# Performance work log

Hardware: AMD Instinct MI355X
Metric: run time of the kernel (lower is better)

The kernel has to match this reference:

```python
import jax, jax.numpy as jnp
import numpy as np

N, E, IN, HID, OUT, H = 50000, 400000, 128, 32, 64, 4
HID_DIM = HID * H  # 128


def _param(key, shape, scale=0.05):
    return jax.random.normal(key, shape, dtype=jnp.float32) * scale


def setup_inputs() -> dict:
    key = jax.random.key(0)
    ks = jax.random.split(key, 32)
    inp = {
        "x": jax.random.normal(ks[0], (N, IN), dtype=jnp.float32),
        "edge_index": jax.random.randint(ks[1], (2, E), 0, N, dtype=jnp.int32),
        "edge_weight": jax.random.uniform(ks[2], (E,), dtype=jnp.float32),
        # layer 0: in=128 -> H=4, C=32, concat => 128
        "Wl0": _param(ks[3], (IN, H * HID)), "bl0": jnp.zeros((H * HID,), jnp.float32),
        "Wr0": _param(ks[4], (IN, H * HID)), "br0": jnp.zeros((H * HID,), jnp.float32),
        "We0": _param(ks[5], (1, H * HID)),
        "att0": _param(ks[6], (H, HID)),
        "b0": jnp.zeros((H * HID,), jnp.float32),
        "g0": jnp.ones((H * HID,), jnp.float32), "be0": jnp.zeros((H * HID,), jnp.float32),
        # layer 1: in=128 -> H=4, C=64, concat=False (mean over heads) => 64
        "Wl1": _param(ks[7], (HID_DIM, H * OUT)), "bl1": jnp.zeros((H * OUT,), jnp.float32),
        "Wr1": _param(ks[8], (HID_DIM, H * OUT)), "br1": jnp.zeros((H * OUT,), jnp.float32),
        "We1": _param(ks[9], (1, H * OUT)),
        "att1": _param(ks[10], (H, OUT)),
        "b1": jnp.zeros((OUT,), jnp.float32),
        "g1": jnp.ones((OUT,), jnp.float32), "be1": jnp.zeros((OUT,), jnp.float32),
        # residual projections
        "P0": _param(ks[11], (IN, HID_DIM)), "pb0": jnp.zeros((HID_DIM,), jnp.float32),
        "P1": _param(ks[12], (HID_DIM, OUT)), "pb1": jnp.zeros((OUT,), jnp.float32),
    }
    return inp


def _add_self_loops(src, dst, ew):
    # PyG add_self_loops with fill_value='mean': loop attr = mean of incoming edge attrs per node
    s = jax.ops.segment_sum(ew, dst, num_segments=N)
    cnt = jax.ops.segment_sum(jnp.ones_like(ew), dst, num_segments=N)
    loop_w = s / jnp.maximum(cnt, 1.0)
    idx = jnp.arange(N, dtype=src.dtype)
    return jnp.concatenate([src, idx]), jnp.concatenate([dst, idx]), jnp.concatenate([ew, loop_w])


def _gatv2_layer(x, src, dst, ew, Wl, bl, Wr, br, We, att, b, g, be, C, concat):
    xl = (x @ Wl + bl).reshape(N, H, C)  # source transform (lin_l)
    xr = (x @ Wr + br).reshape(N, H, C)  # target transform (lin_r)
    eattr = (ew[:, None] @ We).reshape(-1, H, C)
    e = jax.nn.leaky_relu(xl[src] + xr[dst] + eattr, 0.2)  # [E', H, C]
    logits = jnp.einsum('ehc,hc->eh', e, att)
    # segment softmax over target nodes
    m = jax.ops.segment_max(logits, dst, num_segments=N)
    p = jnp.exp(logits - m[dst])
    denom = jax.ops.segment_sum(p, dst, num_segments=N)
    alpha = p / denom[dst]
    out = jax.ops.segment_sum(xl[src] * alpha[..., None], dst, num_segments=N)  # [N, H, C]
    if concat:
        out = out.reshape(N, H * C) + b
    else:
        out = out.mean(axis=1) + b
    out = jax.nn.elu(out)
    mu = out.mean(-1, keepdims=True)
    var = out.var(-1, keepdims=True)
    return (out - mu) / jnp.sqrt(var + 1e-5) * g + be


def reference(x, edge_index, edge_weight,
              Wl0, bl0, Wr0, br0, We0, att0, b0, g0, be0,
              Wl1, bl1, Wr1, br1, We1, att1, b1, g1, be1,
              P0, pb0, P1, pb1):
    src, dst, ew = _add_self_loops(edge_index[0], edge_index[1], edge_weight)
    h = x
    h1 = _gatv2_layer(h, src, dst, ew, Wl0, bl0, Wr0, br0, We0, att0, b0, g0, be0, HID, True)
    h = h1 + (h @ P0 + pb0)
    h2 = _gatv2_layer(h, src, dst, ew, Wl1, bl1, Wr1, br1, We1, att1, b1, g1, be1, OUT, False)
    h = h2 + (h @ P1 + pb1)
    return h
```

## Files before the change

### kernel.cpp

```cpp
#include <hip/hip_runtime.h>
#include <math.h>

#define N_NODES 50000
#define N_EDGES 400000
#define NPAD    50176
#define MROWS   50048
#define HC0 128
#define HC1 256

typedef short bf16x8 __attribute__((ext_vector_type(8)));
typedef float f32x4  __attribute__((ext_vector_type(4)));

__device__ inline unsigned short f2bf(float f) {
  union { float f; unsigned u; } v; v.f = f;
  unsigned r = v.u + 0x7FFFu + ((v.u >> 16) & 1u);
  return (unsigned short)(r >> 16);
}
__device__ inline float bf2f(unsigned short h) {
  union { unsigned u; float f; } v; v.u = ((unsigned)h) << 16;
  return v.f;
}

__global__ void deg_kernel(const int* __restrict__ ei, const float* __restrict__ ew,
                           float* __restrict__ s, int* __restrict__ deg) {
  int e = blockIdx.x * 256 + threadIdx.x;
  if (e < N_EDGES) {
    int dst = ei[N_EDGES + e];
    atomicAdd(&s[dst], ew[e]);
    atomicAdd(&deg[dst], 1);
  }
}

__global__ void loopw_kernel(float* __restrict__ s, const int* __restrict__ deg) {
  int i = blockIdx.x * 256 + threadIdx.x;
  if (i < N_NODES) s[i] = s[i] / fmaxf((float)deg[i], 1.0f);
}

__global__ void scan1(const int* __restrict__ deg, int* __restrict__ part,
                      int* __restrict__ bsum) {
  int i = blockIdx.x * 256 + threadIdx.x;
  int lane = threadIdx.x & 63, wid = threadIdx.x >> 6;
  int v = deg[i];
  int inc = v;
#pragma unroll
  for (int d = 1; d < 64; d <<= 1) { int y = __shfl_up(inc, d, 64); if (lane >= d) inc += y; }
  __shared__ int wsum[4];
  if (lane == 63) wsum[wid] = inc;
  __syncthreads();
  int off = 0;
#pragma unroll
  for (int w = 0; w < 4; ++w) { int sv = wsum[w]; if (w < wid) off += sv; }
  part[i] = inc - v + off;
  if (threadIdx.x == 0) bsum[blockIdx.x] = wsum[0] + wsum[1] + wsum[2] + wsum[3];
}

__global__ void scan2(int* __restrict__ bsum) {
  int t = threadIdx.x;
  int lane = t & 63, wid = t >> 6;
  int v = (t < 196) ? bsum[t] : 0;
  int inc = v;
#pragma unroll
  for (int d = 1; d < 64; d <<= 1) { int y = __shfl_up(inc, d, 64); if (lane >= d) inc += y; }
  __shared__ int wsum[4];
  if (lane == 63) wsum[wid] = inc;
  __syncthreads();
  int off = 0;
#pragma unroll
  for (int w = 0; w < 4; ++w) { int sv = wsum[w]; if (w < wid) off += sv; }
  if (t < 196) bsum[t] = inc - v + off;
}

__global__ void scatter_kernel(const int* __restrict__ ei, const float* __restrict__ ew,
                               const int* __restrict__ part, const int* __restrict__ bsum,
                               int* __restrict__ cursor,
                               int* __restrict__ csrc, float* __restrict__ cw) {
  int e = blockIdx.x * 256 + threadIdx.x;
  if (e >= N_EDGES) return;
  int dst = ei[N_EDGES + e];
  int pos = atomicAdd(&cursor[dst], 1);
  int idx = part[dst] + bsum[dst >> 8] + pos;
  csrc[idx] = ei[e];
  cw[idx]  = ew[e];
}

__global__ void cvt_bf16(const float* __restrict__ in, unsigned short* __restrict__ out,
                         int n4) {
  int i = blockIdx.x * 256 + threadIdx.x;
  if (i >= n4) return;
  float4 v = ((const float4*)in)[i];
  ushort4 o; o.x = f2bf(v.x); o.y = f2bf(v.y); o.z = f2bf(v.z); o.w = f2bf(v.w);
  ((ushort4*)out)[i] = o;
}

__global__ void pack_w(const float* __restrict__ Wl0, const float* __restrict__ Wr0,
                       const float* __restrict__ P0,  const float* __restrict__ Wl1,
                       const float* __restrict__ Wr1, const float* __restrict__ P1,
                       unsigned short* __restrict__ o_wl0, unsigned short* __restrict__ o_wr0,
                       unsigned short* __restrict__ o_p0,  unsigned short* __restrict__ o_wl1,
                       unsigned short* __restrict__ o_wr1, unsigned short* __restrict__ o_p1) {
  int n = blockIdx.x, k = threadIdx.x;
  const float* W; unsigned short* O; int N, nl;
  if      (n < 128) { W = Wl0; O = o_wl0; N = 128; nl = n; }
  else if (n < 256) { W = Wr0; O = o_wr0; N = 128; nl = n - 128; }
  else if (n < 384) { W = P0;  O = o_p0;  N = 128; nl = n - 256; }
  else if (n < 640) { W = Wl1; O = o_wl1; N = 256; nl = n - 384; }
  else if (n < 896) { W = Wr1; O = o_wr1; N = 256; nl = n - 640; }
  else              { W = P1;  O = o_p1;  N = 64;  nl = n - 896; }
  O[nl * 128 + k] = f2bf(W[(size_t)k * N + nl]);
}

__global__ __launch_bounds__(256) void gemm_l0(
    const unsigned short* __restrict__ A, const unsigned short* __restrict__ BT,
    const float* __restrict__ bias0, const float* __restrict__ bias1,
    const float* __restrict__ bias2,
    unsigned short* __restrict__ o_xl, unsigned short* __restrict__ o_xr,
    float* __restrict__ o_h, int M) {
  __shared__ unsigned short As[64 * 136];
  const int tid = threadIdx.x;
  const int rbase = blockIdx.x * 64;
#pragma unroll
  for (int i = 0; i < 4; ++i) {
    int c = i * 256 + tid;
    int row = c >> 4, slot = c & 15;
    int ar = rbase + row; if (ar > M - 1) ar = M - 1;
    uint4 v = *(const uint4*)(A + (size_t)ar * 128 + slot * 8);
    *(uint4*)(As + row * 136 + slot * 8) = v;
  }
  __syncthreads();
  const int w = tid >> 6, l = tid & 63;
  const int lr = l & 15, lg = l >> 4;
#pragma unroll
  for (int i = 0; i < 6; ++i) {
    const int ct = w * 6 + i;
    const bf16x8* bp = (const bf16x8*)(BT + (size_t)(ct * 16 + lr) * 128 + lg * 8);
    bf16x8 b0 = bp[0], b1 = bp[4], b2 = bp[8], b3 = bp[12];
    const int colb = ct * 16 + lg * 4;
    const int cc = colb & 127;
    const float* bptr = (ct < 8 ? bias0 : (ct < 16 ? bias1 : bias2));
    float4 bv = *(const float4*)(bptr + cc);
#pragma unroll
    for (int rt = 0; rt < 4; ++rt) {
      const unsigned short* ap = As + (rt * 16 + lr) * 136 + lg * 8;
      bf16x8 a0 = *(const bf16x8*)(ap);
      bf16x8 a1 = *(const bf16x8*)(ap + 32);
      bf16x8 a2 = *(const bf16x8*)(ap + 64);
      bf16x8 a3 = *(const bf16x8*)(ap + 96);
      f32x4 acc = {0.f, 0.f, 0.f, 0.f};
      acc = __builtin_amdgcn_mfma_f32_16x16x32_bf16(b0, a0, acc, 0, 0, 0);
      acc = __builtin_amdgcn_mfma_f32_16x16x32_bf16(b1, a1, acc, 0, 0, 0);
      acc = __builtin_amdgcn_mfma_f32_16x16x32_bf16(b2, a2, acc, 0, 0, 0);
      acc = __builtin_amdgcn_mfma_f32_16x16x32_bf16(b3, a3, acc, 0, 0, 0);
      const int row = rbase + rt * 16 + lr;
      if (ct < 16) {
        ushort4 o;
        o.x = f2bf(acc[0] + bv.x); o.y = f2bf(acc[1] + bv.y);
        o.z = f2bf(acc[2] + bv.z); o.w = f2bf(acc[3] + bv.w);
        *(ushort4*)((ct < 8 ? o_xl : o_xr) + (size_t)row * 128 + cc) = o;
      } else {
        float4 o;
        o.x = acc[0] + bv.x; o.y = acc[1] + bv.y;
        o.z = acc[2] + bv.z; o.w = acc[3] + bv.w;
        *(float4*)(o_h + (size_t)row * 128 + cc) = o;
      }
    }
  }
}

__global__ __launch_bounds__(256) void gemm_l1(
    const unsigned short* __restrict__ A, const unsigned short* __restrict__ BT,
    const float* __restrict__ bias0, const float* __restrict__ bias1,
    const float* __restrict__ bias2,
    unsigned short* __restrict__ o_xl, unsigned short* __restrict__ o_xr,
    float* __restrict__ o_out, int M) {
  __shared__ unsigned short As[64 * 136];
  const int tid = threadIdx.x;
  const int rbase = blockIdx.x * 64;
#pragma unroll
  for (int i = 0; i < 4; ++i) {
    int c = i * 256 + tid;
    int row = c >> 4, slot = c & 15;
    int ar = rbase + row; if (ar > M - 1) ar = M - 1;
    uint4 v = *(const uint4*)(A + (size_t)ar * 128 + slot * 8);
    *(uint4*)(As + row * 136 + slot * 8) = v;
  }
  __syncthreads();
  const int w = tid >> 6, l = tid & 63;
  const int lr = l & 15, lg = l >> 4;
#pragma unroll
  for (int i = 0; i < 9; ++i) {
    const int ct = w * 9 + i;
    const bf16x8* bp = (const bf16x8*)(BT + (size_t)(ct * 16 + lr) * 128 + lg * 8);
    bf16x8 b0 = bp[0], b1 = bp[4], b2 = bp[8], b3 = bp[12];
    const int colb = ct * 16 + lg * 4;
    const int cc = (ct < 32) ? (colb & 255) : (colb - 512);
    const float* bptr = (ct < 16 ? bias0 : (ct < 32 ? bias1 : bias2));
    float4 bv = *(const float4*)(bptr + cc);
#pragma unroll
    for (int rt = 0; rt < 4; ++rt) {
      const unsigned short* ap = As + (rt * 16 + lr) * 136 + lg * 8;
      bf16x8 a0 = *(const bf16x8*)(ap);
      bf16x8 a1 = *(const bf16x8*)(ap + 32);
      bf16x8 a2 = *(const bf16x8*)(ap + 64);
      bf16x8 a3 = *(const bf16x8*)(ap + 96);
      f32x4 acc = {0.f, 0.f, 0.f, 0.f};
      acc = __builtin_amdgcn_mfma_f32_16x16x32_bf16(b0, a0, acc, 0, 0, 0);
      acc = __builtin_amdgcn_mfma_f32_16x16x32_bf16(b1, a1, acc, 0, 0, 0);
      acc = __builtin_amdgcn_mfma_f32_16x16x32_bf16(b2, a2, acc, 0, 0, 0);
      acc = __builtin_amdgcn_mfma_f32_16x16x32_bf16(b3, a3, acc, 0, 0, 0);
      const int row = rbase + rt * 16 + lr;
      if (ct < 32) {
        ushort4 o;
        o.x = f2bf(acc[0] + bv.x); o.y = f2bf(acc[1] + bv.y);
        o.z = f2bf(acc[2] + bv.z); o.w = f2bf(acc[3] + bv.w);
        *(ushort4*)((ct < 16 ? o_xl : o_xr) + (size_t)row * 256 + cc) = o;
      } else if (row < M) {
        float4 o;
        o.x = acc[0] + bv.x; o.y = acc[1] + bv.y;
        o.z = acc[2] + bv.z; o.w = acc[3] + bv.w;
        *(float4*)(o_out + (size_t)row * 64 + cc) = o;
      }
    }
  }
}

__global__ __launch_bounds__(256) void agg0(
    const int* __restrict__ part, const int* __restrict__ bsum,
    const int* __restrict__ deg, const int* __restrict__ csrc,
    const float* __restrict__ cw, const float* __restrict__ loop_w,
    const unsigned short* __restrict__ xl, const unsigned short* __restrict__ xr,
    const float* __restrict__ We, const float* __restrict__ att,
    const float* __restrict__ b, const float* __restrict__ g,
    const float* __restrict__ be, const float* __restrict__ hres,
    unsigned short* __restrict__ hout) {
  const int wid = threadIdx.x >> 6, l = threadIdx.x & 63;
  const int n = blockIdx.x * 4 + wid;
  const int grp = l >> 4, cl = l & 15, c0 = cl * 8;
  float xrv[8], wef[8], attf[8];
  {
    bf16x8 x8 = *(const bf16x8*)(xr + (size_t)n * HC0 + c0);
    float4 w0 = *(const float4*)(We + c0),  w1 = *(const float4*)(We + c0 + 4);
    float4 t0 = *(const float4*)(att + c0), t1 = *(const float4*)(att + c0 + 4);
    wef[0]=w0.x; wef[1]=w0.y; wef[2]=w0.z; wef[3]=w0.w;
    wef[4]=w1.x; wef[5]=w1.y; wef[6]=w1.z; wef[7]=w1.w;
    attf[0]=t0.x; attf[1]=t0.y; attf[2]=t0.z; attf[3]=t0.w;
    attf[4]=t1.x; attf[5]=t1.y; attf[6]=t1.z; attf[7]=t1.w;
#pragma unroll
    for (int j = 0; j < 8; ++j) xrv[j] = bf2f((unsigned short)x8[j]);
  }
  const int start = part[n] + bsum[n >> 8];
  const int cnt   = deg[n] + 1;
  float acc[8] = {0,0,0,0,0,0,0,0}, den = 0.f;
  const int iters = (cnt + 3) >> 2;
  for (int kk = 0; kk < iters; ++kk) {
    int e = kk * 4 + grp;
    bool valid = e < cnt;
    int src; float w;
    if (e == 0)      { src = n; w = loop_w[n]; }
    else if (valid)  { src = csrc[start + e - 1]; w = cw[start + e - 1]; }
    else             { src = n; w = 0.f; }
    bf16x8 a8 = *(const bf16x8*)(xl + (size_t)src * HC0 + c0);
    float av[8], c = 0.f;
#pragma unroll
    for (int j = 0; j < 8; ++j) {
      av[j] = bf2f((unsigned short)a8[j]);
      float sv = av[j] + xrv[j] + w * wef[j];
      float lk = fmaxf(sv, 0.2f * sv);
      c = fmaf(lk, attf[j], c);
    }
    c += __shfl_xor(c, 1, 64); c += __shfl_xor(c, 2, 64);
    float p = valid ? __expf(c) : 0.f;
    den += p;
#pragma unroll
    for (int j = 0; j < 8; ++j) acc[j] = fmaf(p, av[j], acc[j]);
  }
  den += __shfl_xor(den, 16, 64); den += __shfl_xor(den, 32, 64);
#pragma unroll
  for (int j = 0; j < 8; ++j) {
    acc[j] += __shfl_xor(acc[j], 16, 64);
    acc[j] += __shfl_xor(acc[j], 32, 64);
  }
  float v[8], s1 = 0.f, s2 = 0.f;
  float dinv = 1.f / den;
  {
    float4 b0v = *(const float4*)(b + c0), b1v = *(const float4*)(b + c0 + 4);
    float bb[8] = {b0v.x,b0v.y,b0v.z,b0v.w,b1v.x,b1v.y,b1v.z,b1v.w};
#pragma unroll
    for (int j = 0; j < 8; ++j) {
      float t = acc[j] * dinv + bb[j];
      t = t > 0.f ? t : __expf(t) - 1.f;
      v[j] = t; s1 += t; s2 += t * t;
    }
  }
  s1 += __shfl_xor(s1, 1, 64); s2 += __shfl_xor(s2, 1, 64);
  s1 += __shfl_xor(s1, 2, 64); s2 += __shfl_xor(s2, 2, 64);
  s1 += __shfl_xor(s1, 4, 64); s2 += __shfl_xor(s2, 4, 64);
  s1 += __shfl_xor(s1, 8, 64); s2 += __shfl_xor(s2, 8, 64);
  float mean = s1 * (1.f / 128.f);
  float inv  = rsqrtf(s2 * (1.f / 128.f) - mean * mean + 1e-5f);
  if (grp == 0) {
    float4 g0v = *(const float4*)(g + c0),  g1v = *(const float4*)(g + c0 + 4);
    float4 e0v = *(const float4*)(be + c0), e1v = *(const float4*)(be + c0 + 4);
    float4 h0v = *(const float4*)(hres + (size_t)n * HC0 + c0);
    float4 h1v = *(const float4*)(hres + (size_t)n * HC0 + c0 + 4);
    float gg[8] = {g0v.x,g0v.y,g0v.z,g0v.w,g1v.x,g1v.y,g1v.z,g1v.w};
    float ee[8] = {e0v.x,e0v.y,e0v.z,e0v.w,e1v.x,e1v.y,e1v.z,e1v.w};
    float hh[8] = {h0v.x,h0v.y,h0v.z,h0v.w,h1v.x,h1v.y,h1v.z,h1v.w};
    bf16x8 o;
#pragma unroll
    for (int j = 0; j < 8; ++j)
      o[j] = (short)f2bf((v[j] - mean) * inv * gg[j] + ee[j] + hh[j]);
    *(bf16x8*)(hout + (size_t)n * HC0 + c0) = o;
  }
}

__global__ __launch_bounds__(256) void agg1(
    const int* __restrict__ part, const int* __restrict__ bsum,
    const int* __restrict__ deg, const int* __restrict__ csrc,
    const float* __restrict__ cw, const float* __restrict__ loop_w,
    const unsigned short* __restrict__ xl, const unsigned short* __restrict__ xr,
    const float* __restrict__ We, const float* __restrict__ att,
    const float* __restrict__ b, const float* __restrict__ g,
    const float* __restrict__ be, float* __restrict__ out) {
  const int wid = threadIdx.x >> 6, l = threadIdx.x & 63;
  const int n = blockIdx.x * 4 + wid;
  const int grp = l >> 5, cl = l & 31, c0 = cl * 8;
  float xrv[8], wef[8], attf[8];
  {
    bf16x8 x8 = *(const bf16x8*)(xr + (size_t)n * HC1 + c0);
    float4 w0 = *(const float4*)(We + c0),  w1 = *(const float4*)(We + c0 + 4);
    float4 t0 = *(const float4*)(att + c0), t1 = *(const float4*)(att + c0 + 4);
    wef[0]=w0.x; wef[1]=w0.y; wef[2]=w0.z; wef[3]=w0.w;
    wef[4]=w1.x; wef[5]=w1.y; wef[6]=w1.z; wef[7]=w1.w;
    attf[0]=t0.x; attf[1]=t0.y; attf[2]=t0.z; attf[3]=t0.w;
    attf[4]=t1.x; attf[5]=t1.y; attf[6]=t1.z; attf[7]=t1.w;
#pragma unroll
    for (int j = 0; j < 8; ++j) xrv[j] = bf2f((unsigned short)x8[j]);
  }
  const int start = part[n] + bsum[n >> 8];
  const int cnt   = deg[n] + 1;
  float acc[8] = {0,0,0,0,0,0,0,0}, den = 0.f;
  const int iters = (cnt + 1) >> 1;
  for (int kk = 0; kk < iters; ++kk) {
    int e = kk * 2 + grp;
    bool valid = e < cnt;
    int src; float w;
    if (e == 0)      { src = n; w = loop_w[n]; }
    else if (valid)  { src = csrc[start + e - 1]; w = cw[start + e - 1]; }
    else             { src = n; w = 0.f; }
    bf16x8 a8 = *(const bf16x8*)(xl + (size_t)src * HC1 + c0);
    float av[8], c = 0.f;
#pragma unroll
    for (int j = 0; j < 8; ++j) {
      av[j] = bf2f((unsigned short)a8[j]);
      float sv = av[j] + xrv[j] + w * wef[j];
      float lk = fmaxf(sv, 0.2f * sv);
      c = fmaf(lk, attf[j], c);
    }
    c += __shfl_xor(c, 1, 64); c += __shfl_xor(c, 2, 64); c += __shfl_xor(c, 4, 64);
    float p = valid ? __expf(c) : 0.f;
    den += p;
#pragma unroll
    for (int j = 0; j < 8; ++j) acc[j] = fmaf(p, av[j], acc[j]);
  }
  den += __shfl_xor(den, 32, 64);
#pragma unroll
  for (int j = 0; j < 8; ++j) acc[j] += __shfl_xor(acc[j], 32, 64);
  __shared__ float lds[4][HC1];
  if (grp == 0) {
    float dinv = 1.f / den;
#pragma unroll
    for (int j = 0; j < 8; ++j) lds[wid][c0 + j] = acc[j] * dinv;
  }
  __syncthreads();
  float v = 0.25f * (lds[wid][l] + lds[wid][64 + l] + lds[wid][128 + l] +
                     lds[wid][192 + l]) + b[l];
  v = v > 0.f ? v : __expf(v) - 1.f;
  float s1 = v, s2 = v * v;
#pragma unroll
  for (int o = 32; o > 0; o >>= 1) { s1 += __shfl_xor(s1, o, 64); s2 += __shfl_xor(s2, o, 64); }
  float mean = s1 * (1.f / 64.f);
  float inv  = rsqrtf(s2 * (1.f / 64.f) - mean * mean + 1e-5f);
  out[(size_t)n * 64 + l] += (v - mean) * inv * g[l] + be[l];
}

extern "C" void kernel_launch(void* const* d_in, const int* in_sizes, int n_in,
                              void* d_out, int out_size, void* d_ws, size_t ws_size,
                              hipStream_t stream) {
  const float* x    = (const float*)d_in[0];
  const int*   ei   = (const int*)  d_in[1];
  const float* ew   = (const float*)d_in[2];
  const float* Wl0  = (const float*)d_in[3];
  const float* bl0  = (const float*)d_in[4];
  const float* Wr0  = (const float*)d_in[5];
  const float* br0  = (const float*)d_in[6];
  const float* We0  = (const float*)d_in[7];
  const float* att0 = (const float*)d_in[8];
  const float* b0   = (const float*)d_in[9];
  const float* g0   = (const float*)d_in[10];
  const float* be0  = (const float*)d_in[11];
  const float* Wl1  = (const float*)d_in[12];
  const float* bl1  = (const float*)d_in[13];
  const float* Wr1  = (const float*)d_in[14];
  const float* br1  = (const float*)d_in[15];
  const float* We1  = (const float*)d_in[16];
  const float* att1 = (const float*)d_in[17];
  const float* b1   = (const float*)d_in[18];
  const float* g1   = (const float*)d_in[19];
  const float* be1  = (const float*)d_in[20];
  const float* P0   = (const float*)d_in[21];
  const float* pb0  = (const float*)d_in[22];
  const float* P1   = (const float*)d_in[23];
  const float* pb1  = (const float*)d_in[24];
  float* out = (float*)d_out;

  float* f        = (float*)d_ws;
  float* s_loopw  = f;
  int*   deg      = (int*)(f + 50176);
  int*   cursor   = (int*)(f + 100352);
  int*   part     = (int*)(f + 150528);
  int*   bsum     = (int*)(f + 200704);
  int*   csrc     = (int*)(f + 200960);
  float* cw       = f + 601344;
  unsigned short* wl0T = (unsigned short*)(f + 1001728);
  unsigned short* wr0T = wl0T + 16384;
  unsigned short* p0T  = wl0T + 32768;
  unsigned short* wl1T = (unsigned short*)(f + 1026304);
  unsigned short* wr1T = wl1T + 32768;
  unsigned short* p1T  = wl1T + 65536;
  unsigned short* xb   = (unsigned short*)(f + 1063168);
  unsigned short* hb   = (unsigned short*)(f + 4266240);
  float*          hres = f + 7469312;
  unsigned short* RA   = (unsigned short*)(f + 13875456);
  unsigned short* RB   = (unsigned short*)(f + 20281600);
  unsigned short* xl0b = RA, *xr0b = RB;
  unsigned short* xl1b = RA, *xr1b = RB;

  hipMemsetAsync(s_loopw, 0, (size_t)(50176 * 3) * sizeof(float), stream);
  deg_kernel<<<(N_EDGES + 255) / 256, 256, 0, stream>>>(ei, ew, s_loopw, deg);
  loopw_kernel<<<(N_NODES + 255) / 256, 256, 0, stream>>>(s_loopw, deg);
  scan1<<<NPAD / 256, 256, 0, stream>>>(deg, part, bsum);
  scan2<<<1, 256, 0, stream>>>(bsum);
  scatter_kernel<<<(N_EDGES + 255) / 256, 256, 0, stream>>>(ei, ew, part, bsum,
                                                            cursor, csrc, cw);

  cvt_bf16<<<(N_NODES * 128 / 4 + 255) / 256, 256, 0, stream>>>(x, xb, N_NODES * 128 / 4);
  pack_w<<<960, 128, 0, stream>>>(Wl0, Wr0, P0, Wl1, Wr1, P1,
                                  wl0T, wr0T, p0T, wl1T, wr1T, p1T);

  const int GB = MROWS / 64;
  gemm_l0<<<GB, 256, 0, stream>>>(xb, wl0T, bl0, br0, pb0, xl0b, xr0b, hres, N_NODES);
  agg0<<<N_NODES / 4, 256, 0, stream>>>(part, bsum, deg, csrc, cw, s_loopw,
                                        xl0b, xr0b, We0, att0, b0, g0, be0, hres, hb);

  gemm_l1<<<GB, 256, 0, stream>>>(hb, wl1T, bl1, br1, pb1, xl1b, xr1b, out, N_NODES);
  agg1<<<N_NODES / 4, 256, 0, stream>>>(part, bsum, deg, csrc, cw, s_loopw,
                                        xl1b, xr1b, We1, att1, b1, g1, be1, out);
}
```

Baseline: 262.4 us.

## Pack CSR as int2 records with self-loops inline and prefetch gathers in aggregation

The CSR now stores (src, weight) pairs as interleaved int2 records, with the self-loop entry written into each node's segment by a new self_kernel, which also replaces the separate loop-weight kernel. The aggregation loops in agg0 and agg1 drop the per-edge branching and software-pipeline the edge-record and xl gathers two iterations ahead, processing two edges per trip. The aim is to cut dependent-load latency in the gather-bound aggregation and remove a launch. Out-of-range prefetches are clamped to the last valid index, which adds some redundant loads and register pressure.

```diff
diff --git a/kernel.cpp b/kernel.cpp
--- a/kernel.cpp
+++ b/kernel.cpp
@@ -31,16 +31,11 @@
   }
 }
 
-__global__ void loopw_kernel(float* __restrict__ s, const int* __restrict__ deg) {
-  int i = blockIdx.x * 256 + threadIdx.x;
-  if (i < N_NODES) s[i] = s[i] / fmaxf((float)deg[i], 1.0f);
-}
-
 __global__ void scan1(const int* __restrict__ deg, int* __restrict__ part,
                       int* __restrict__ bsum) {
   int i = blockIdx.x * 256 + threadIdx.x;
   int lane = threadIdx.x & 63, wid = threadIdx.x >> 6;
-  int v = deg[i];
+  int v = (i < N_NODES) ? deg[i] + 1 : 0;
   int inc = v;
 #pragma unroll
   for (int d = 1; d < 64; d <<= 1) { int y = __shfl_up(inc, d, 64); if (lane >= d) inc += y; }
@@ -70,17 +65,25 @@
   if (t < 196) bsum[t] = inc - v + off;
 }
 
+__global__ void self_kernel(const float* __restrict__ s, const int* __restrict__ deg,
+                            const int* __restrict__ part, const int* __restrict__ bsum,
+                            int2* __restrict__ csr2) {
+  int i = blockIdx.x * 256 + threadIdx.x;
+  if (i >= N_NODES) return;
+  float w = s[i] / fmaxf((float)deg[i], 1.0f);
+  int start = part[i] + bsum[i >> 8];
+  csr2[start] = make_int2(i, __float_as_int(w));
+}
+
 __global__ void scatter_kernel(const int* __restrict__ ei, const float* __restrict__ ew,
                                const int* __restrict__ part, const int* __restrict__ bsum,
-                               int* __restrict__ cursor,
-                               int* __restrict__ csrc, float* __restrict__ cw) {
+                               int* __restrict__ cursor, int2* __restrict__ csr2) {
   int e = blockIdx.x * 256 + threadIdx.x;
   if (e >= N_EDGES) return;
   int dst = ei[N_EDGES + e];
   int pos = atomicAdd(&cursor[dst], 1);
-  int idx = part[dst] + bsum[dst >> 8] + pos;
-  csrc[idx] = ei[e];
-  cw[idx]  = ew[e];
+  int idx = part[dst] + bsum[dst >> 8] + 1 + pos;
+  csr2[idx] = make_int2(ei[e], __float_as_int(ew[e]));
 }
 
 __global__ void cvt_bf16(const float* __restrict__ in, unsigned short* __restrict__ out,
@@ -223,10 +226,49 @@
   }
 }
 
+__device__ inline void edge_step0(int2 rec, bf16x8 a8, bool valid,
+                                  const float* xrv, const float* wef, const float* attf,
+                                  float* acc, float& den) {
+  float w = __int_as_float(rec.y);
+  float av[8], c = 0.f;
+#pragma unroll
+  for (int j = 0; j < 8; ++j) {
+    av[j] = bf2f((unsigned short)a8[j]);
+    float t  = fmaf(w, wef[j], xrv[j]);
+    float sv = av[j] + t;
+    float lk = fmaxf(sv, 0.2f * sv);
+    c = fmaf(lk, attf[j], c);
+  }
+  c += __shfl_xor(c, 1, 64); c += __shfl_xor(c, 2, 64);
+  float p = valid ? __expf(c) : 0.f;
+  den += p;
+#pragma unroll
+  for (int j = 0; j < 8; ++j) acc[j] = fmaf(p, av[j], acc[j]);
+}
+
+__device__ inline void edge_step1(int2 rec, bf16x8 a8, bool valid,
+                                  const float* xrv, const float* wef, const float* attf,
+                                  float* acc, float& den) {
+  float w = __int_as_float(rec.y);
+  float av[8], c = 0.f;
+#pragma unroll
+  for (int j = 0; j < 8; ++j) {
+    av[j] = bf2f((unsigned short)a8[j]);
+    float t  = fmaf(w, wef[j], xrv[j]);
+    float sv = av[j] + t;
+    float lk = fmaxf(sv, 0.2f * sv);
+    c = fmaf(lk, attf[j], c);
+  }
+  c += __shfl_xor(c, 1, 64); c += __shfl_xor(c, 2, 64); c += __shfl_xor(c, 4, 64);
+  float p = valid ? __expf(c) : 0.f;
+  den += p;
+#pragma unroll
+  for (int j = 0; j < 8; ++j) acc[j] = fmaf(p, av[j], acc[j]);
+}
+
 __global__ __launch_bounds__(256) void agg0(
     const int* __restrict__ part, const int* __restrict__ bsum,
-    const int* __restrict__ deg, const int* __restrict__ csrc,
-    const float* __restrict__ cw, const float* __restrict__ loop_w,
+    const int* __restrict__ deg, const int2* __restrict__ csr2,
     const unsigned short* __restrict__ xl, const unsigned short* __restrict__ xr,
     const float* __restrict__ We, const float* __restrict__ att,
     const float* __restrict__ b, const float* __restrict__ g,
@@ -249,29 +291,24 @@
   }
   const int start = part[n] + bsum[n >> 8];
   const int cnt   = deg[n] + 1;
+  const int last  = start + cnt - 1;
   float acc[8] = {0,0,0,0,0,0,0,0}, den = 0.f;
-  const int iters = (cnt + 3) >> 2;
-  for (int kk = 0; kk < iters; ++kk) {
-    int e = kk * 4 + grp;
-    bool valid = e < cnt;
-    int src; float w;
-    if (e == 0)      { src = n; w = loop_w[n]; }
-    else if (valid)  { src = csrc[start + e - 1]; w = cw[start + e - 1]; }
-    else             { src = n; w = 0.f; }
-    bf16x8 a8 = *(const bf16x8*)(xl + (size_t)src * HC0 + c0);
-    float av[8], c = 0.f;
-#pragma unroll
-    for (int j = 0; j < 8; ++j) {
-      av[j] = bf2f((unsigned short)a8[j]);
-      float sv = av[j] + xrv[j] + w * wef[j];
-      float lk = fmaxf(sv, 0.2f * sv);
-      c = fmaf(lk, attf[j], c);
-    }
-    c += __shfl_xor(c, 1, 64); c += __shfl_xor(c, 2, 64);
-    float p = valid ? __expf(c) : 0.f;
-    den += p;
-#pragma unroll
-    for (int j = 0; j < 8; ++j) acc[j] = fmaf(p, av[j], acc[j]);
+  int e = grp;
+  int i0 = start + e;     if (i0 > last) i0 = last;
+  int i1 = start + e + 4; if (i1 > last) i1 = last;
+  int2 r0 = csr2[i0], r1 = csr2[i1];
+  bf16x8 a0 = *(const bf16x8*)(xl + (size_t)r0.x * HC0 + c0);
+  bf16x8 a1 = *(const bf16x8*)(xl + (size_t)r1.x * HC0 + c0);
+  const int trips = (cnt + 7) >> 3;
+  for (int t = 0; t < trips; ++t) {
+    int i2 = start + e + 8;  if (i2 > last) i2 = last;
+    int i3 = start + e + 12; if (i3 > last) i3 = last;
+    int2 r2 = csr2[i2], r3 = csr2[i3];
+    bf16x8 p2 = *(const bf16x8*)(xl + (size_t)r2.x * HC0 + c0);
+    bf16x8 p3 = *(const bf16x8*)(xl + (size_t)r3.x * HC0 + c0);
+    edge_step0(r0, a0, e < cnt,     xrv, wef, attf, acc, den);
+    edge_step0(r1, a1, e + 4 < cnt, xrv, wef, attf, acc, den);
+    r0 = r2; r1 = r3; a0 = p2; a1 = p3; e += 8;
   }
   den += __shfl_xor(den, 16, 64); den += __shfl_xor(den, 32, 64);
 #pragma unroll
@@ -315,8 +352,7 @@
 
 __global__ __launch_bounds__(256) void agg1(
     const int* __restrict__ part, const int* __restrict__ bsum,
-    const int* __restrict__ deg, const int* __restrict__ csrc,
-    const float* __restrict__ cw, const float* __restrict__ loop_w,
+    const int* __restrict__ deg, const int2* __restrict__ csr2,
     const unsigned short* __restrict__ xl, const unsigned short* __restrict__ xr,
     const float* __restrict__ We, const float* __restrict__ att,
     const float* __restrict__ b, const float* __restrict__ g,
@@ -338,29 +374,24 @@
   }
   const int start = part[n] + bsum[n >> 8];
   const int cnt   = deg[n] + 1;
+  const int last  = start + cnt - 1;
   float acc[8] = {0,0,0,0,0,0,0,0}, den = 0.f;
-  const int iters = (cnt + 1) >> 1;
-  for (int kk = 0; kk < iters; ++kk) {
-    int e = kk * 2 + grp;
-    bool valid = e < cnt;
-    int src; float w;
-    if (e == 0)      { src = n; w = loop_w[n]; }
-    else if (valid)  { src = csrc[start + e - 1]; w = cw[start + e - 1]; }
-    else             { src = n; w = 0.f; }
-    bf16x8 a8 = *(const bf16x8*)(xl + (size_t)src * HC1 + c0);
-    float av[8], c = 0.f;
-#pragma unroll
-    for (int j = 0; j < 8; ++j) {
-      av[j] = bf2f((unsigned short)a8[j]);
-      float sv = av[j] + xrv[j] + w * wef[j];
-      float lk = fmaxf(sv, 0.2f * sv);
-      c = fmaf(lk, attf[j], c);
-    }
-    c += __shfl_xor(c, 1, 64); c += __shfl_xor(c, 2, 64); c += __shfl_xor(c, 4, 64);
-    float p = valid ? __expf(c) : 0.f;
-    den += p;
-#pragma unroll
-    for (int j = 0; j < 8; ++j) acc[j] = fmaf(p, av[j], acc[j]);
+  int e = grp;
+  int i0 = start + e;     if (i0 > last) i0 = last;
+  int i1 = start + e + 2; if (i1 > last) i1 = last;
+  int2 r0 = csr2[i0], r1 = csr2[i1];
+  bf16x8 a0 = *(const bf16x8*)(xl + (size_t)r0.x * HC1 + c0);
+  bf16x8 a1 = *(const bf16x8*)(xl + (size_t)r1.x * HC1 + c0);
+  const int trips = (cnt + 3) >> 2;
+  for (int t = 0; t < trips; ++t) {
+    int i2 = start + e + 4; if (i2 > last) i2 = last;
+    int i3 = start + e + 6; if (i3 > last) i3 = last;
+    int2 r2 = csr2[i2], r3 = csr2[i3];
+    bf16x8 p2 = *(const bf16x8*)(xl + (size_t)r2.x * HC1 + c0);
+    bf16x8 p3 = *(const bf16x8*)(xl + (size_t)r3.x * HC1 + c0);
+    edge_step1(r0, a0, e < cnt,     xrv, wef, attf, acc, den);
+    edge_step1(r1, a1, e + 2 < cnt, xrv, wef, attf, acc, den);
+    r0 = r2; r1 = r3; a0 = p2; a1 = p3; e += 4;
   }
   den += __shfl_xor(den, 32, 64);
 #pragma unroll
@@ -419,29 +450,28 @@
   int*   cursor   = (int*)(f + 100352);
   int*   part     = (int*)(f + 150528);
   int*   bsum     = (int*)(f + 200704);
-  int*   csrc     = (int*)(f + 200960);
-  float* cw       = f + 601344;
-  unsigned short* wl0T = (unsigned short*)(f + 1001728);
+  int2*  csr2     = (int2*)(f + 200960);
+  unsigned short* wl0T = (unsigned short*)(f + 1102080);
   unsigned short* wr0T = wl0T + 16384;
   unsigned short* p0T  = wl0T + 32768;
-  unsigned short* wl1T = (unsigned short*)(f + 1026304);
+  unsigned short* wl1T = (unsigned short*)(f + 1126656);
   unsigned short* wr1T = wl1T + 32768;
   unsigned short* p1T  = wl1T + 65536;
-  unsigned short* xb   = (unsigned short*)(f + 1063168);
-  unsigned short* hb   = (unsigned short*)(f + 4266240);
-  float*          hres = f + 7469312;
-  unsigned short* RA   = (unsigned short*)(f + 13875456);
-  unsigned short* RB   = (unsigned short*)(f + 20281600);
+  unsigned short* xb   = (unsigned short*)(f + 1163520);
+  unsigned short* hb   = (unsigned short*)(f + 4366592);
+  float*          hres = f + 7569664;
+  unsigned short* RA   = (unsigned short*)(f + 13975808);
+  unsigned short* RB   = (unsigned short*)(f + 20381952);
   unsigned short* xl0b = RA, *xr0b = RB;
   unsigned short* xl1b = RA, *xr1b = RB;
 
   hipMemsetAsync(s_loopw, 0, (size_t)(50176 * 3) * sizeof(float), stream);
   deg_kernel<<<(N_EDGES + 255) / 256, 256, 0, stream>>>(ei, ew, s_loopw, deg);
-  loopw_kernel<<<(N_NODES + 255) / 256, 256, 0, stream>>>(s_loopw, deg);
   scan1<<<NPAD / 256, 256, 0, stream>>>(deg, part, bsum);
   scan2<<<1, 256, 0, stream>>>(bsum);
+  self_kernel<<<(N_NODES + 255) / 256, 256, 0, stream>>>(s_loopw, deg, part, bsum, csr2);
   scatter_kernel<<<(N_EDGES + 255) / 256, 256, 0, stream>>>(ei, ew, part, bsum,
-                                                            cursor, csrc, cw);
+                                                            cursor, csr2);
 
   cvt_bf16<<<(N_NODES * 128 / 4 + 255) / 256, 256, 0, stream>>>(x, xb, N_NODES * 128 / 4);
   pack_w<<<960, 128, 0, stream>>>(Wl0, Wr0, P0, Wl1, Wr1, P1,
@@ -449,10 +479,10 @@
 
   const int GB = MROWS / 64;
   gemm_l0<<<GB, 256, 0, stream>>>(xb, wl0T, bl0, br0, pb0, xl0b, xr0b, hres, N_NODES);
-  agg0<<<N_NODES / 4, 256, 0, stream>>>(part, bsum, deg, csrc, cw, s_loopw,
+  agg0<<<N_NODES / 4, 256, 0, stream>>>(part, bsum, deg, csr2,
                                         xl0b, xr0b, We0, att0, b0, g0, be0, hres, hb);
 
   gemm_l1<<<GB, 256, 0, stream>>>(hb, wl1T, bl1, br1, pb1, xl1b, xr1b, out, N_NODES);
-  agg1<<<N_NODES / 4, 256, 0, stream>>>(part, bsum, deg, csrc, cw, s_loopw,
+  agg1<<<N_NODES / 4, 256, 0, stream>>>(part, bsum, deg, csr2,
                                         xl1b, xr1b, We1, att1, b1, g1, be1, out);
 }
```

Result: faster. 247.3 us (-5.7%).
